# Performance work log

Hardware: AMD Instinct MI355X
Metric: run time of the kernel (lower is better)

The kernel has to match this reference:

```python
import jax, jax.numpy as jnp
import numpy as np

NEG_INF = -1e9  # module uses -1e9 negativeInfinity constant
BS, DA, SL, H = 16, 512, 1024, 8


def setup_inputs() -> dict:
    key = jax.random.key(0)
    ks = jax.random.split(key, 8)
    return {
        "q":    jax.random.normal(ks[0], (BS, DA, SL), dtype=jnp.float32),
        "k_in": jax.random.normal(ks[1], (BS, DA, SL), dtype=jnp.float32),
        "v_in": jax.random.normal(ks[2], (BS, DA, SL), dtype=jnp.float32),
        "k_w":  jax.random.normal(ks[3], (DA, DA), dtype=jnp.float32) * 0.05,
        "k_b":  jax.random.normal(ks[4], (DA,), dtype=jnp.float32) * 0.05,
        "v_w":  jax.random.normal(ks[5], (DA, DA), dtype=jnp.float32) * 0.05,
        "v_b":  jax.random.normal(ks[6], (DA,), dtype=jnp.float32) * 0.05,
        "gbn_gamma": jnp.ones((H,), dtype=jnp.float32),
        "gbn_bias":  jnp.zeros((H,), dtype=jnp.float32),
        "gbn_m":     jnp.zeros((H,), dtype=jnp.float32),
        "gbn_s":     jnp.ones((H,), dtype=jnp.float32),
        "mask": jax.random.randint(ks[7], (BS, 1, 1, SL), 0, 2, dtype=jnp.int32),
    }


def reference(q, k_in, v_in, k_w, k_b, v_w, v_b, gbn_gamma, gbn_bias, gbn_m, gbn_s, mask):
    bs, da, qsl = q.shape
    h = gbn_gamma.shape[0]
    dh = da // h
    sl = k_in.shape[2]
    mask_b = mask.astype(bool)                 # [bs,1,1,sl] True = masked

    # 1x1 conv1d projections == per-position matmul over channels
    k = jnp.einsum('ok,bks->bos', k_w, k_in) + k_b[None, :, None]   # [bs,da,sl]
    v = jnp.einsum('ov,bvs->bos', v_w, v_in) + v_b[None, :, None]   # [bs,dva,sl]
    dva = v.shape[1]
    dvh = dva // h

    qh = q.reshape(bs, h, dh, qsl).transpose(0, 1, 3, 2)   # [bs,h,qsl,dh]
    kh = k.reshape(bs, h, dh, sl)                          # [bs,h,dh,sl]
    vh = v.reshape(bs, h, dvh, sl).transpose(0, 1, 3, 2)   # [bs,h,sl,dvh]

    scores = jnp.einsum('bhqd,bhds->bhqs', qh, kh)         # [bs,h,qsl,sl]

    # GhostBatchNorm1d(features=h) in eval mode: per-head affine normalization
    scores = (scores - gbn_m[None, :, None, None]) / gbn_s[None, :, None, None]
    scores = scores * gbn_gamma[None, :, None, None] + gbn_bias[None, :, None, None]

    mask_k = mask_b                           # [bs,1,1,sl]  mask key positions (selfAttention fill)
    mask_q = jnp.swapaxes(mask_b, 2, 3)       # [bs,1,sl,1]  mask query rows (transposed fill)
    scores = jnp.where(mask_k, NEG_INF, scores)
    scores = jnp.where(mask_q, NEG_INF, scores)

    w = jax.nn.softmax(scores, axis=-1)
    w = jnp.where(mask_q, 0.0, w)             # v_weights.masked_fill(mask, 0)

    out = jnp.einsum('bhqs,bhsd->bhqd', w, vh)             # [bs,h,qsl,dvh]
    out = out.transpose(0, 1, 3, 2).reshape(bs, dva, qsl)  # back to channels-first
    return out
```

## Files before the change

### kernel.cpp

```cpp
#include <hip/hip_runtime.h>

typedef _Float16 f16;
typedef _Float16 h8_t __attribute__((ext_vector_type(8)));
typedef _Float16 h4_t __attribute__((ext_vector_type(4)));
typedef float f32x4 __attribute__((ext_vector_type(4)));
typedef float f32x16 __attribute__((ext_vector_type(16)));

#define BS 16
#define DA 512
#define SL 1024
#define NH 8
#define DH 64

template <int MODE>
__global__ __launch_bounds__(256) void fused_proj(const float* __restrict__ Wg,
                                                  const float* __restrict__ Xin,
                                                  const float* __restrict__ bias,
                                                  f16* __restrict__ outg) {
  constexpr int MT = MODE ? SL : DA;
  constexpr int NT = MODE ? DA : SL;
  __shared__ f16 Wl[128 * 40];
  __shared__ f16 Xl[128 * 40];
  __shared__ float Xf32[32 * 132];
  const int b = blockIdx.z;
  const int m0 = blockIdx.x * 128;
  const int n0 = blockIdx.y * 128;
  const int o_base = MODE ? n0 : m0;
  const int s_base = MODE ? m0 : n0;
  const int t = threadIdx.x;
  const int w = t >> 6, lane = t & 63, lr = lane & 15, lq = lane >> 4;
  const int wm = (w >> 1) * 64, wn = (w & 1) * 64;

  f32x4 acc[4][4] = {};

  for (int kt = 0; kt < 16; ++kt) {
    const int c0 = kt * 32;
    __syncthreads();
#pragma unroll
    for (int p = 0; p < 4; ++p) {
      const int idx = p * 256 + t;
      const int row = idx >> 3, cq = (idx & 7) * 4;
      const float4 v = *(const float4*)&Wg[(size_t)(o_base + row) * DA + c0 + cq];
      h4_t hv;
      hv[0] = (f16)v.x; hv[1] = (f16)v.y; hv[2] = (f16)v.z; hv[3] = (f16)v.w;
      *(h4_t*)&Wl[row * 40 + cq] = hv;
    }
#pragma unroll
    for (int p = 0; p < 4; ++p) {
      const int idx = p * 256 + t;
      const int cc = idx >> 5, s4 = (idx & 31) * 4;
      const float4 v = *(const float4*)&Xin[((size_t)b * DA + c0 + cc) * SL + s_base + s4];
      *(float4*)&Xf32[cc * 132 + s4] = v;
    }
    __syncthreads();
    {
      const int srow = t >> 1, cb = (t & 1) * 16;
      h8_t lo, hi;
#pragma unroll
      for (int u = 0; u < 8; ++u) lo[u] = (f16)Xf32[(cb + u) * 132 + srow];
#pragma unroll
      for (int u = 0; u < 8; ++u) hi[u] = (f16)Xf32[(cb + 8 + u) * 132 + srow];
      *(h8_t*)&Xl[srow * 40 + cb] = lo;
      *(h8_t*)&Xl[srow * 40 + cb + 8] = hi;
    }
    __syncthreads();
    const f16* Al = MODE ? Xl : Wl;
    const f16* Bl = MODE ? Wl : Xl;
    h8_t af[4], bf[4];
#pragma unroll
    for (int i = 0; i < 4; ++i) af[i] = *(const h8_t*)&Al[(wm + i * 16 + lr) * 40 + lq * 8];
#pragma unroll
    for (int j = 0; j < 4; ++j) bf[j] = *(const h8_t*)&Bl[(wn + j * 16 + lr) * 40 + lq * 8];
#pragma unroll
    for (int i = 0; i < 4; ++i)
#pragma unroll
      for (int j = 0; j < 4; ++j)
        acc[i][j] = __builtin_amdgcn_mfma_f32_16x16x32_f16(af[i], bf[j], acc[i][j], 0, 0, 0);
  }

#pragma unroll
  for (int i = 0; i < 4; ++i) {
    const int gmb = m0 + wm + i * 16 + lq * 4;
    float bm[4] = {0.f, 0.f, 0.f, 0.f};
    if (MODE == 0) {
      const float4 b4 = *(const float4*)&bias[gmb];
      bm[0] = b4.x; bm[1] = b4.y; bm[2] = b4.z; bm[3] = b4.w;
    }
#pragma unroll
    for (int j = 0; j < 4; ++j) {
      const int gn = n0 + wn + j * 16 + lr;
      const float bn = (MODE == 1) ? bias[gn] : 0.f;
      h4_t hv;
#pragma unroll
      for (int r = 0; r < 4; ++r) {
        const float val = acc[i][j][r] + (MODE == 0 ? bm[r] : bn);
        hv[r] = (f16)val;
      }
      *(h4_t*)&outg[((size_t)b * NT + gn) * MT + gmb] = hv;
    }
  }
}

__global__ __launch_bounds__(256, 2) void attn_kernel(
    const float* __restrict__ qg, const f16* __restrict__ kp, const f16* __restrict__ vp,
    const float* __restrict__ gamma, const float* __restrict__ gbns,
    const int* __restrict__ maskg, float* __restrict__ outg) {
  __shared__ __align__(16) char smem[36864];
  f16* KV = (f16*)smem;
  float* Osh = (float*)smem;

  const int bh = blockIdx.x, b = bh >> 3, h = bh & 7;
  const int i0 = blockIdx.y * 256;
  const int t = threadIdx.x, w = t >> 6, lane = t & 63;
  const int l5 = lane & 31, hf = lane >> 5;
  const float scale = gamma[h] / gbns[h] * 1.44269504088896f;

  h8_t qf[2][4];
#pragma unroll
  for (int im = 0; im < 2; ++im)
#pragma unroll
    for (int ks = 0; ks < 4; ++ks) {
      h8_t v;
#pragma unroll
      for (int u = 0; u < 8; ++u) {
        const int d = ks * 16 + hf * 8 + u;
        v[u] = (f16)(qg[((size_t)b * DA + h * DH + d) * SL + i0 + w * 64 + im * 32 + l5] * scale);
      }
      qf[im][ks] = v;
    }

  const int srow = t >> 3;
  const int c8 = (t & 7) * 8;

  uint4 rk[2], rv[2];
#pragma unroll
  for (int p = 0; p < 2; ++p) {
    const int row = p * 32 + srow;
    rk[p] = *(const uint4*)&kp[((size_t)b * SL + row) * DA + h * DH + c8];
    rv[p] = *(const uint4*)&vp[((size_t)b * DA + h * DH + row) * SL + c8];
  }
  {
    f16* K0 = KV;
    f16* V0 = KV + 4608;
#pragma unroll
    for (int p = 0; p < 2; ++p) {
      const int row = p * 32 + srow;
      const int rowp = (row & ~12) | ((row & 4) << 1) | ((row & 8) >> 1);
      *(uint4*)&K0[rowp * 72 + c8] = rk[p];
      *(uint4*)&V0[row * 72 + c8] = rv[p];
    }
  }
  __syncthreads();

  float m_i[2] = {-3e38f, -3e38f}, l_i[2] = {0.f, 0.f};
  f32x16 acc[2][2] = {};

  for (int jt = 0; jt < 16; ++jt) {
    const int j0 = jt * 64;
    const f16* Kc = KV + (jt & 1) * 9216;
    const f16* Vc = Kc + 4608;

    if (jt < 15) {
      const int jn = j0 + 64;
#pragma unroll
      for (int p = 0; p < 2; ++p) {
        const int row = p * 32 + srow;
        rk[p] = *(const uint4*)&kp[((size_t)b * SL + jn + row) * DA + h * DH + c8];
        rv[p] = *(const uint4*)&vp[((size_t)b * DA + h * DH + row) * SL + jn + c8];
      }
    }
    int4 mq[2][4];
#pragma unroll
    for (int mj = 0; mj < 2; ++mj)
#pragma unroll
      for (int q = 0; q < 4; ++q)
        mq[mj][q] = *(const int4*)&maskg[b * SL + j0 + mj * 32 + (q >> 1) * 16 + hf * 8 + (q & 1) * 4];

    f32x16 sa[2][2] = {};
#pragma unroll
    for (int ks = 0; ks < 4; ++ks)
#pragma unroll
      for (int mj = 0; mj < 2; ++mj) {
        const h8_t kf = *(const h8_t*)&Kc[(mj * 32 + l5) * 72 + ks * 16 + hf * 8];
#pragma unroll
        for (int im = 0; im < 2; ++im)
          sa[im][mj] = __builtin_amdgcn_mfma_f32_32x32x16_f16(kf, qf[im][ks], sa[im][mj], 0, 0, 0);
      }

#pragma unroll
    for (int mj = 0; mj < 2; ++mj)
#pragma unroll
      for (int q = 0; q < 4; ++q) {
        const int4 m4 = mq[mj][q];
#pragma unroll
        for (int im = 0; im < 2; ++im) {
          if (m4.x) sa[im][mj][q * 4 + 0] = -1e9f;
          if (m4.y) sa[im][mj][q * 4 + 1] = -1e9f;
          if (m4.z) sa[im][mj][q * 4 + 2] = -1e9f;
          if (m4.w) sa[im][mj][q * 4 + 3] = -1e9f;
        }
      }

    float alpha[2];
#pragma unroll
    for (int im = 0; im < 2; ++im) {
      float mx = sa[im][0][0];
#pragma unroll
      for (int e = 1; e < 16; ++e) mx = fmaxf(mx, sa[im][0][e]);
#pragma unroll
      for (int e = 0; e < 16; ++e) mx = fmaxf(mx, sa[im][1][e]);
      mx = fmaxf(mx, __shfl_xor(mx, 32));
      const float mn = fmaxf(m_i[im], mx);
      alpha[im] = __builtin_amdgcn_exp2f(m_i[im] - mn);
      m_i[im] = mn;
      float rs = 0.f;
#pragma unroll
      for (int mj = 0; mj < 2; ++mj)
#pragma unroll
        for (int e = 0; e < 16; ++e) {
          const float pv = __builtin_amdgcn_exp2f(sa[im][mj][e] - mn);
          sa[im][mj][e] = pv;
          rs += pv;
        }
      rs += __shfl_xor(rs, 32);
      l_i[im] = l_i[im] * alpha[im] + rs;
#pragma unroll
      for (int nd = 0; nd < 2; ++nd)
#pragma unroll
        for (int e = 0; e < 16; ++e) acc[im][nd][e] *= alpha[im];
    }

#pragma unroll
    for (int jk = 0; jk < 4; ++jk) {
      const int mj = jk >> 1, g = jk & 1;
      h8_t pf[2];
#pragma unroll
      for (int im = 0; im < 2; ++im) {
        h8_t pk;
#pragma unroll
        for (int u = 0; u < 8; ++u) pk[u] = (f16)sa[im][mj][g * 8 + u];
        pf[im] = pk;
      }
#pragma unroll
      for (int nd = 0; nd < 2; ++nd) {
        const h8_t vf = *(const h8_t*)&Vc[(nd * 32 + l5) * 72 + jk * 16 + hf * 8];
#pragma unroll
        for (int im = 0; im < 2; ++im)
          acc[im][nd] = __builtin_amdgcn_mfma_f32_32x32x16_f16(vf, pf[im], acc[im][nd], 0, 0, 0);
      }
    }

    if (jt < 15) {
      f16* Kn = KV + ((jt + 1) & 1) * 9216;
      f16* Vn = Kn + 4608;
#pragma unroll
      for (int p = 0; p < 2; ++p) {
        const int row = p * 32 + srow;
        const int rowp = (row & ~12) | ((row & 4) << 1) | ((row & 8) >> 1);
        *(uint4*)&Kn[rowp * 72 + c8] = rk[p];
        *(uint4*)&Vn[row * 72 + c8] = rv[p];
      }
      __syncthreads();
    }
  }

  float fac[2];
#pragma unroll
  for (int im = 0; im < 2; ++im) {
    const int mo = maskg[b * SL + i0 + w * 64 + im * 32 + l5];
    fac[im] = mo ? 0.f : 1.f / l_i[im];
  }
  __syncthreads();

#pragma unroll
  for (int nd = 0; nd < 2; ++nd) {
#pragma unroll
    for (int im = 0; im < 2; ++im)
#pragma unroll
      for (int e = 0; e < 16; ++e) {
        const int dl = (e & 3) + 8 * (e >> 2) + 4 * hf;
        Osh[dl * 256 + w * 64 + im * 32 + l5] = acc[im][nd][e] * fac[im];
      }
    __syncthreads();
#pragma unroll
    for (int pass = 0; pass < 8; ++pass) {
      const int row = pass * 4 + w;
      const int i4 = lane * 4;
      const float4 o = *(const float4*)&Osh[row * 256 + i4];
      *(float4*)&outg[((size_t)b * DA + h * DH + nd * 32 + row) * SL + i0 + i4] = o;
    }
    __syncthreads();
  }
}

extern "C" void kernel_launch(void* const* d_in, const int* in_sizes, int n_in,
                              void* d_out, int out_size, void* d_ws, size_t ws_size,
                              hipStream_t stream) {
  const float* q     = (const float*)d_in[0];
  const float* k_in  = (const float*)d_in[1];
  const float* v_in  = (const float*)d_in[2];
  const float* k_w   = (const float*)d_in[3];
  const float* k_b   = (const float*)d_in[4];
  const float* v_w   = (const float*)d_in[5];
  const float* v_b   = (const float*)d_in[6];
  const float* gamma = (const float*)d_in[7];
  const float* gbns  = (const float*)d_in[10];
  const int*   mask  = (const int*)d_in[11];
  float* out = (float*)d_out;

  const size_t NEL = (size_t)BS * SL * DA;
  f16* kpw = (f16*)d_ws;
  f16* vpw = kpw + NEL;

  fused_proj<0><<<dim3(4, 8, BS), 256, 0, stream>>>(k_w, k_in, k_b, kpw);
  fused_proj<1><<<dim3(8, 4, BS), 256, 0, stream>>>(v_w, v_in, v_b, vpw);
  attn_kernel<<<dim3(BS * NH, SL / 256), 256, 0, stream>>>(q, kpw, vpw, gamma, gbns, mask, out);
}
```

Before: 261.7 us.

## Split projections into fp16 transpose-prep pass and direct-to-LDS GEMMs

```diff
diff --git a/kernel.cpp b/kernel.cpp
--- a/kernel.cpp
+++ b/kernel.cpp
@@ -11,6 +11,128 @@
 #define SL 1024
 #define NH 8
 #define DH 64
+
+__device__ __forceinline__ void gload_lds16(const void* g, void* l) {
+  __builtin_amdgcn_global_load_lds((const __attribute__((address_space(1))) void*)g,
+                                   (__attribute__((address_space(3))) void*)l, 16, 0, 0);
+}
+
+__global__ __launch_bounds__(256) void prep_kernel(
+    const float* __restrict__ k_in, const float* __restrict__ v_in,
+    const float* __restrict__ k_w, const float* __restrict__ v_w,
+    f16* __restrict__ Kt, f16* __restrict__ Vt,
+    f16* __restrict__ kwh, f16* __restrict__ vwh) {
+  const int blk = blockIdx.x;
+  const int t = threadIdx.x;
+  if (blk < 2048) {
+    const int which = blk >> 10;
+    const int r = blk & 1023;
+    const int b = r >> 6;
+    const int c0 = ((r >> 3) & 7) * 64;
+    const int s0 = (r & 7) * 128;
+    const float* src = which ? v_in : k_in;
+    f16* dst = which ? Vt : Kt;
+    __shared__ __align__(16) float Xf32[64 * 132];
+#pragma unroll
+    for (int p = 0; p < 8; ++p) {
+      const int idx = p * 256 + t;
+      const int cc = idx >> 5, s4 = (idx & 31) * 4;
+      const float4 v = *(const float4*)&src[((size_t)b * DA + c0 + cc) * SL + s0 + s4];
+      *(float4*)&Xf32[cc * 132 + s4] = v;
+    }
+    __syncthreads();
+    const int srow = t >> 1, cb = (t & 1) * 32;
+#pragma unroll
+    for (int g = 0; g < 4; ++g) {
+      h8_t h;
+#pragma unroll
+      for (int u = 0; u < 8; ++u) h[u] = (f16)Xf32[(cb + g * 8 + u) * 132 + srow];
+      *(h8_t*)&dst[((size_t)b * SL + s0 + srow) * DA + c0 + cb + g * 8] = h;
+    }
+  } else {
+    const int r = blk - 2048;
+    const int wsel = r >> 5;
+    const float* src = wsel ? v_w : k_w;
+    f16* dst = wsel ? vwh : kwh;
+    const int base = (r & 31) * 8192;
+#pragma unroll
+    for (int p = 0; p < 4; ++p) {
+      const int i = base + p * 2048 + t * 8;
+      const float4 a = *(const float4*)&src[i];
+      const float4 c = *(const float4*)&src[i + 4];
+      h8_t h;
+      h[0] = (f16)a.x; h[1] = (f16)a.y; h[2] = (f16)a.z; h[3] = (f16)a.w;
+      h[4] = (f16)c.x; h[5] = (f16)c.y; h[6] = (f16)c.z; h[7] = (f16)c.w;
+      *(h8_t*)&dst[i] = h;
+    }
+  }
+}
+
+template <int MODE>
+__global__ __launch_bounds__(256) void proj_gemm(const f16* __restrict__ Ag,
+                                                 const f16* __restrict__ Bg,
+                                                 const float* __restrict__ bias,
+                                                 f16* __restrict__ outg) {
+  constexpr int MT = MODE ? SL : DA;
+  constexpr int NT = MODE ? DA : SL;
+  __shared__ __align__(16) f16 Al[128 * 32];
+  __shared__ __align__(16) f16 Bl[128 * 32];
+  const int b = blockIdx.z;
+  const int m0 = blockIdx.x * 128, n0 = blockIdx.y * 128;
+  const int t = threadIdx.x;
+  const int lane = t & 63, w = t >> 6, lr = lane & 15, lq = lane >> 4;
+  const int wm = (w >> 1) * 64, wn = (w & 1) * 64;
+
+  const f16* Arow = Ag + (MODE ? (size_t)b * SL * DA : 0) + (size_t)m0 * DA;
+  const f16* Brow = Bg + (MODE ? 0 : (size_t)b * SL * DA) + (size_t)n0 * DA;
+
+  const int rr = t >> 2;
+  const int c8 = (t & 3) * 8;
+
+  f32x4 acc[4][4] = {};
+
+  for (int kt = 0; kt < 16; ++kt) {
+    const int c0 = kt * 32;
+    __syncthreads();
+    gload_lds16(Arow + (size_t)rr * DA + c0 + c8, Al + t * 8);
+    gload_lds16(Arow + (size_t)(64 + rr) * DA + c0 + c8, Al + 2048 + t * 8);
+    gload_lds16(Brow + (size_t)rr * DA + c0 + c8, Bl + t * 8);
+    gload_lds16(Brow + (size_t)(64 + rr) * DA + c0 + c8, Bl + 2048 + t * 8);
+    __syncthreads();
+    h8_t af[4], bf[4];
+#pragma unroll
+    for (int i = 0; i < 4; ++i) af[i] = *(const h8_t*)&Al[(wm + i * 16 + lr) * 32 + lq * 8];
+#pragma unroll
+    for (int j = 0; j < 4; ++j) bf[j] = *(const h8_t*)&Bl[(wn + j * 16 + lr) * 32 + lq * 8];
+#pragma unroll
+    for (int i = 0; i < 4; ++i)
+#pragma unroll
+      for (int j = 0; j < 4; ++j)
+        acc[i][j] = __builtin_amdgcn_mfma_f32_16x16x32_f16(af[i], bf[j], acc[i][j], 0, 0, 0);
+  }
+
+#pragma unroll
+  for (int i = 0; i < 4; ++i) {
+    const int gmb = m0 + wm + i * 16 + lq * 4;
+    float bm[4] = {0.f, 0.f, 0.f, 0.f};
+    if (MODE == 0) {
+      const float4 b4 = *(const float4*)&bias[gmb];
+      bm[0] = b4.x; bm[1] = b4.y; bm[2] = b4.z; bm[3] = b4.w;
+    }
+#pragma unroll
+    for (int j = 0; j < 4; ++j) {
+      const int gn = n0 + wn + j * 16 + lr;
+      const float bn = (MODE == 1) ? bias[gn] : 0.f;
+      h4_t hv;
+#pragma unroll
+      for (int r = 0; r < 4; ++r) {
+        const float val = acc[i][j][r] + (MODE == 0 ? bm[r] : bn);
+        hv[r] = (f16)val;
+      }
+      *(h4_t*)&outg[((size_t)b * NT + gn) * MT + gmb] = hv;
+    }
+  }
+}
 
 template <int MODE>
 __global__ __launch_bounds__(256) void fused_proj(const float* __restrict__ Wg,
@@ -64,13 +186,13 @@
       *(h8_t*)&Xl[srow * 40 + cb + 8] = hi;
     }
     __syncthreads();
-    const f16* Al = MODE ? Xl : Wl;
-    const f16* Bl = MODE ? Wl : Xl;
+    const f16* Alp = MODE ? Xl : Wl;
+    const f16* Blp = MODE ? Wl : Xl;
     h8_t af[4], bf[4];
 #pragma unroll
-    for (int i = 0; i < 4; ++i) af[i] = *(const h8_t*)&Al[(wm + i * 16 + lr) * 40 + lq * 8];
-#pragma unroll
-    for (int j = 0; j < 4; ++j) bf[j] = *(const h8_t*)&Bl[(wn + j * 16 + lr) * 40 + lq * 8];
+    for (int i = 0; i < 4; ++i) af[i] = *(const h8_t*)&Alp[(wm + i * 16 + lr) * 40 + lq * 8];
+#pragma unroll
+    for (int j = 0; j < 4; ++j) bf[j] = *(const h8_t*)&Blp[(wn + j * 16 + lr) * 40 + lq * 8];
 #pragma unroll
     for (int i = 0; i < 4; ++i)
 #pragma unroll
@@ -312,7 +434,18 @@
   f16* kpw = (f16*)d_ws;
   f16* vpw = kpw + NEL;
 
-  fused_proj<0><<<dim3(4, 8, BS), 256, 0, stream>>>(k_w, k_in, k_b, kpw);
-  fused_proj<1><<<dim3(8, 4, BS), 256, 0, stream>>>(v_w, v_in, v_b, vpw);
+  const size_t need = NEL * 2 * 4 + (size_t)DA * DA * 2 * 2;
+  if (ws_size >= need) {
+    f16* Kt  = vpw + NEL;
+    f16* Vt  = Kt + NEL;
+    f16* kwh = Vt + NEL;
+    f16* vwh = kwh + (size_t)DA * DA;
+    prep_kernel<<<dim3(2112), 256, 0, stream>>>(k_in, v_in, k_w, v_w, Kt, Vt, kwh, vwh);
+    proj_gemm<0><<<dim3(4, 8, BS), 256, 0, stream>>>(kwh, Kt, k_b, kpw);
+    proj_gemm<1><<<dim3(8, 4, BS), 256, 0, stream>>>(Vt, vwh, v_b, vpw);
+  } else {
+    fused_proj<0><<<dim3(4, 8, BS), 256, 0, stream>>>(k_w, k_in, k_b, kpw);
+    fused_proj<1><<<dim3(8, 4, BS), 256, 0, stream>>>(v_w, v_in, v_b, vpw);
+  }
   attn_kernel<<<dim3(BS * NH, SL / 256), 256, 0, stream>>>(q, kpw, vpw, gamma, gbns, mask, out);
 }
```

Result: faster. 255.9 us (-2.2%).
